# Performance work log

Measured on AMD Instinct MI355X. Metric: run time of the kernel, lower is better.

## Reference

```python
import jax, jax.numpy as jnp
import numpy as np

N, E, IN, H, OUT, K = 50000, 800000, 128, 64, 64, 1024


def setup_inputs() -> dict:
    key = jax.random.key(0)
    ks = jax.random.split(key, 8)
    x = jax.random.normal(ks[0], (N, IN), dtype=jnp.float32)
    edge_index = jax.random.randint(ks[1], (2, E), 0, N, dtype=jnp.int32)
    cluster_id = jax.random.randint(ks[2], (N,), 0, K, dtype=jnp.int32)
    W1 = jax.random.normal(ks[3], (IN, H), dtype=jnp.float32) / np.float32(np.sqrt(IN))
    b1 = jnp.zeros((H,), jnp.float32)
    W2 = jax.random.normal(ks[4], (H, OUT), dtype=jnp.float32) / np.float32(np.sqrt(H))
    b2 = jnp.zeros((OUT,), jnp.float32)
    W_skip = jax.random.normal(ks[5], (H, OUT), dtype=jnp.float32) / np.float32(np.sqrt(H))
    b_skip = jnp.zeros((OUT,), jnp.float32)
    alpha = jnp.full((1,), 1.5, jnp.float32)
    return dict(x=x, edge_index=edge_index, cluster_id=cluster_id, W1=W1, b1=b1,
                W2=W2, b2=b2, W_skip=W_skip, b_skip=b_skip, alpha=alpha)


def gcn_conv_sparse(x, src, dst, n, W, b):
    # PyG GCNConv: transform, then D^{-1/2}(A+I)D^{-1/2} aggregation, then bias.
    h = x @ W  # [n, F_out]
    deg = jax.ops.segment_sum(jnp.ones_like(src, dtype=h.dtype), dst, num_segments=n) + 1.0
    dinv = jax.lax.rsqrt(deg)
    norm = dinv[src] * dinv[dst]  # [E]
    agg = jax.ops.segment_sum(h[src] * norm[:, None], dst, num_segments=n)
    agg = agg + (dinv * dinv)[:, None] * h  # self-loop term
    return agg + b


def reference(x, edge_index, cluster_id, W1, b1, W2, b2, W_skip, b_skip, alpha):
    src, dst = edge_index[0], edge_index[1]
    # conv1 + ReLU (dropout is identity in eval mode)
    x1 = jax.nn.relu(gcn_conv_sparse(x, src, dst, N, W1, b1))  # [N, H]

    # pool_by_partition: scatter-mean node features into K clusters
    sums = jax.ops.segment_sum(x1, cluster_id, num_segments=K)  # [K, H]
    counts = jnp.maximum(jax.ops.segment_sum(jnp.ones((N,), x1.dtype), cluster_id, num_segments=K), 1.0)
    x_p = sums / counts[:, None]

    # deduped pooled edges, self-loops removed == dense 0/1 adjacency with zero diag (K small)
    cu, cv = cluster_id[src], cluster_id[dst]
    A = jnp.zeros((K, K), x1.dtype).at[cu, cv].set(1.0)
    A = A * (1.0 - jnp.eye(K, dtype=x1.dtype))
    A_hat = A + jnp.eye(K, dtype=x1.dtype)
    deg_p = jnp.sum(A_hat, axis=0)  # in-degree at target (PyG computes deg on col)
    dinv_p = jax.lax.rsqrt(deg_p)
    A_norm = dinv_p[:, None] * A_hat * dinv_p[None, :]  # [src, dst]
    h_p = x_p @ W2
    x_p2 = jnp.einsum('st,sf->tf', A_norm, h_p) + b2  # [K, OUT]

    # gather-broadcast + strengthened skip head
    up = x_p2[cluster_id]  # [N, OUT]
    skip = x1 @ W_skip + b_skip
    logits = up + jax.nn.relu(alpha)[0] * skip
    return logits
```

## Files before the change

kernel.cpp:

```cpp
#include <hip/hip_runtime.h>

#define NN 50000
#define NE 800000
#define FIN 128
#define FH 64
#define FOUT 64
#define KC 1024
#define CAP 64

typedef unsigned char  u8;
typedef unsigned short u16;
typedef unsigned int   u32;

__global__ __launch_bounds__(256) void k_edge(const int* __restrict__ src,
                                              const int* __restrict__ dst,
                                              const int* __restrict__ cid,
                                              int* __restrict__ deg,
                                              u16* __restrict__ slots,
                                              u8* __restrict__ AT) {
    int e = blockIdx.x * 256 + threadIdx.x;
    if (e >= NE) return;
    int s = src[e], d = dst[e];
    int pos = atomicAdd(&deg[d], 1);
    if (pos < CAP) slots[(size_t)d * CAP + pos] = (u16)s;
    int cu = cid[s], cv = cid[d];
    if (cu != cv) AT[(size_t)cv * KC + cu] = 1;
}

__global__ __launch_bounds__(256) void k_degp(const u8* __restrict__ AT,
                                              float* __restrict__ dinvp) {
    __shared__ int sm[4];
    int t = blockIdx.x;
    int lane = threadIdx.x & 63, w = threadIdx.x >> 6;
    const u32* row = (const u32*)(AT + (size_t)t * KC);
    int s = __popc(row[threadIdx.x]);
    for (int o = 32; o; o >>= 1) s += __shfl_down(s, o);
    if (lane == 0) sm[w] = s;
    __syncthreads();
    if (threadIdx.x == 0)
        dinvp[t] = rsqrtf(1.0f + (float)(sm[0] + sm[1] + sm[2] + sm[3]));
}

__global__ __launch_bounds__(256) void k_node(const int* __restrict__ deg,
                                              const int* __restrict__ cid,
                                              float* __restrict__ dinv,
                                              int* __restrict__ counts) {
    int i = blockIdx.x * 256 + threadIdx.x;
    if (i >= NN) return;
    dinv[i] = rsqrtf((float)deg[i] + 1.0f);
    atomicAdd(&counts[cid[i]], 1);
}

__global__ __launch_bounds__(256) void k_gemm1(const float* __restrict__ x,
                                               const float* __restrict__ W1,
                                               const float* __restrict__ dinv,
                                               float* __restrict__ h) {
    __shared__ float Ws[FIN * FH];
    __shared__ float Xs[32 * FIN];
    int t = threadIdx.x;
    int row_base = blockIdx.x * 32;
    for (int i = t; i < FIN * FH; i += 256) Ws[i] = W1[i];
    {
        const float4* x4 = (const float4*)x;
        float4* xs4 = (float4*)Xs;
        for (int i = t; i < 32 * 32; i += 256) {
            int r = i >> 5, k4 = i & 31;
            int row = row_base + r;
            float4 v = make_float4(0.f, 0.f, 0.f, 0.f);
            if (row < NN) v = x4[(size_t)row * 32 + k4];
            xs4[i] = v;
        }
    }
    __syncthreads();
    int col = t & 31, grp = t >> 5;
    int r0 = grp * 4;
    const float4* p0 = (const float4*)&Xs[(r0 + 0) * FIN];
    const float4* p1 = (const float4*)&Xs[(r0 + 1) * FIN];
    const float4* p2 = (const float4*)&Xs[(r0 + 2) * FIN];
    const float4* p3 = (const float4*)&Xs[(r0 + 3) * FIN];
    float acc00 = 0.f, acc01 = 0.f, acc10 = 0.f, acc11 = 0.f;
    float acc20 = 0.f, acc21 = 0.f, acc30 = 0.f, acc31 = 0.f;
#pragma unroll 2
    for (int k4 = 0; k4 < FIN / 4; ++k4) {
        float4 a0 = p0[k4], a1 = p1[k4], a2 = p2[k4], a3 = p3[k4];
        const float* wp = &Ws[(k4 * 4) * FH + col];
        float w00 = wp[0],          w01 = wp[32];
        float w10 = wp[FH],         w11 = wp[FH + 32];
        float w20 = wp[2 * FH],     w21 = wp[2 * FH + 32];
        float w30 = wp[3 * FH],     w31 = wp[3 * FH + 32];
        acc00 = fmaf(a0.x, w00, fmaf(a0.y, w10, fmaf(a0.z, w20, fmaf(a0.w, w30, acc00))));
        acc01 = fmaf(a0.x, w01, fmaf(a0.y, w11, fmaf(a0.z, w21, fmaf(a0.w, w31, acc01))));
        acc10 = fmaf(a1.x, w00, fmaf(a1.y, w10, fmaf(a1.z, w20, fmaf(a1.w, w30, acc10))));
        acc11 = fmaf(a1.x, w01, fmaf(a1.y, w11, fmaf(a1.z, w21, fmaf(a1.w, w31, acc11))));
        acc20 = fmaf(a2.x, w00, fmaf(a2.y, w10, fmaf(a2.z, w20, fmaf(a2.w, w30, acc20))));
        acc21 = fmaf(a2.x, w01, fmaf(a2.y, w11, fmaf(a2.z, w21, fmaf(a2.w, w31, acc21))));
        acc30 = fmaf(a3.x, w00, fmaf(a3.y, w10, fmaf(a3.z, w20, fmaf(a3.w, w30, acc30))));
        acc31 = fmaf(a3.x, w01, fmaf(a3.y, w11, fmaf(a3.z, w21, fmaf(a3.w, w31, acc31))));
    }
    int row0 = row_base + r0;
    if (row0 + 0 < NN) { float di = dinv[row0 + 0]; h[(size_t)(row0 + 0) * FH + col] = di * acc00; h[(size_t)(row0 + 0) * FH + col + 32] = di * acc01; }
    if (row0 + 1 < NN) { float di = dinv[row0 + 1]; h[(size_t)(row0 + 1) * FH + col] = di * acc10; h[(size_t)(row0 + 1) * FH + col + 32] = di * acc11; }
    if (row0 + 2 < NN) { float di = dinv[row0 + 2]; h[(size_t)(row0 + 2) * FH + col] = di * acc20; h[(size_t)(row0 + 2) * FH + col + 32] = di * acc21; }
    if (row0 + 3 < NN) { float di = dinv[row0 + 3]; h[(size_t)(row0 + 3) * FH + col] = di * acc30; h[(size_t)(row0 + 3) * FH + col + 32] = di * acc31; }
}

__global__ __launch_bounds__(256) void k_gather(const int* __restrict__ deg,
                                                const u16* __restrict__ slots,
                                                const float* __restrict__ dinv,
                                                const float* __restrict__ h,
                                                const float* __restrict__ b1,
                                                const int* __restrict__ cid,
                                                float* __restrict__ x1,
                                                float* __restrict__ sums) {
    int lane = threadIdx.x & 63;
    int node = blockIdx.x * 4 + (threadIdx.x >> 6);
    if (node >= NN) return;
    int q = lane >> 4, fl = lane & 15;
    const float4* h4 = (const float4*)h;
    int cnt_all = min(deg[node], CAP);
    const u16* cp = slots + (size_t)node * CAP;
    float4 acc = make_float4(0.f, 0.f, 0.f, 0.f);
    {
        int cnt = cnt_all;
        int s = (lane < cnt) ? (int)cp[lane] : 0;
        int nFull = cnt >> 2;
        for (int j = 0; j < nFull; ++j) {
            int ss = __shfl(s, j * 4 + q);
            float4 hv = h4[(size_t)ss * 16 + fl];
            acc.x += hv.x; acc.y += hv.y; acc.z += hv.z; acc.w += hv.w;
        }
        int tail = cnt & 3;
        if (tail) {
            int ss = __shfl(s, nFull * 4 + q);
            float m = (q < tail) ? 1.f : 0.f;
            float4 hv = h4[(size_t)ss * 16 + fl];
            acc.x = fmaf(m, hv.x, acc.x);
            acc.y = fmaf(m, hv.y, acc.y);
            acc.z = fmaf(m, hv.z, acc.z);
            acc.w = fmaf(m, hv.w, acc.w);
        }
    }
    acc.x += __shfl_xor(acc.x, 16); acc.y += __shfl_xor(acc.y, 16);
    acc.z += __shfl_xor(acc.z, 16); acc.w += __shfl_xor(acc.w, 16);
    acc.x += __shfl_xor(acc.x, 32); acc.y += __shfl_xor(acc.y, 32);
    acc.z += __shfl_xor(acc.z, 32); acc.w += __shfl_xor(acc.w, 32);
    float di = dinv[node];
    float4 hs = h4[(size_t)node * 16 + fl];
    const float4* b14 = (const float4*)b1;
    float4 bb = b14[fl];
    float4 v;
    v.x = fmaxf(fmaf(di, acc.x + hs.x, bb.x), 0.f);
    v.y = fmaxf(fmaf(di, acc.y + hs.y, bb.y), 0.f);
    v.z = fmaxf(fmaf(di, acc.z + hs.z, bb.z), 0.f);
    v.w = fmaxf(fmaf(di, acc.w + hs.w, bb.w), 0.f);
    if (q == 0) ((float4*)x1)[(size_t)node * 16 + fl] = v;
    int c = cid[node];
    float comp = (q == 0) ? v.x : (q == 1) ? v.y : (q == 2) ? v.z : v.w;
    unsafeAtomicAdd(&sums[(size_t)c * FH + fl * 4 + q], comp);
}

__global__ __launch_bounds__(64) void k_pool(const float* __restrict__ sums,
                                             const int* __restrict__ counts,
                                             const float* __restrict__ W2,
                                             const float* __restrict__ dinvp,
                                             float* __restrict__ g) {
    __shared__ float xp[FH];
    int s = blockIdx.x, f = threadIdx.x;
    float cnt = fmaxf((float)counts[s], 1.0f);
    xp[f] = sums[(size_t)s * FH + f] / cnt;
    __syncthreads();
    float acc = 0.f;
    for (int j = 0; j < FH; ++j) acc = fmaf(xp[j], W2[j * FH + f], acc);
    g[(size_t)s * FH + f] = dinvp[s] * acc;
}

__global__ __launch_bounds__(256) void k_xp2(const u8* __restrict__ AT,
                                             const float* __restrict__ g,
                                             const float* __restrict__ dinvp,
                                             const float* __restrict__ b2,
                                             float* __restrict__ xp2) {
    __shared__ float4 sm4[4][16];
    int t = blockIdx.x;
    int lane = threadIdx.x & 63, w = threadIdx.x >> 6;
    int q = lane >> 4, fl = lane & 15;
    const u32* roww = (const u32*)(AT + (size_t)t * KC);
    const float4* g4 = (const float4*)g;
    float4 acc = make_float4(0.f, 0.f, 0.f, 0.f);
    int wb = w * 64;
    u32 wv = roww[wb + lane];
    for (int j = 0; j < 16; ++j) {
        u32 word = __shfl((int)wv, j * 4 + q);
        int sidx = (wb + j * 4 + q) * 4;
#pragma unroll
        for (int b = 0; b < 4; ++b) {
            float a = (float)((word >> (8 * b)) & 255u);
            float4 gv = g4[(size_t)(sidx + b) * 16 + fl];
            acc.x = fmaf(a, gv.x, acc.x);
            acc.y = fmaf(a, gv.y, acc.y);
            acc.z = fmaf(a, gv.z, acc.z);
            acc.w = fmaf(a, gv.w, acc.w);
        }
    }
    acc.x += __shfl_xor(acc.x, 16); acc.y += __shfl_xor(acc.y, 16);
    acc.z += __shfl_xor(acc.z, 16); acc.w += __shfl_xor(acc.w, 16);
    acc.x += __shfl_xor(acc.x, 32); acc.y += __shfl_xor(acc.y, 32);
    acc.z += __shfl_xor(acc.z, 32); acc.w += __shfl_xor(acc.w, 32);
    if (q == 0) sm4[w][fl] = acc;
    __syncthreads();
    if (threadIdx.x < 16) {
        int f = threadIdx.x;
        float4 a0 = sm4[0][f], a1 = sm4[1][f], a2 = sm4[2][f], a3 = sm4[3][f];
        float4 gs = g4[(size_t)t * 16 + f];
        float dp = dinvp[t];
        const float4* b24 = (const float4*)b2;
        float4 bb = b24[f];
        float4 o;
        o.x = fmaf(dp, a0.x + a1.x + a2.x + a3.x + gs.x, bb.x);
        o.y = fmaf(dp, a0.y + a1.y + a2.y + a3.y + gs.y, bb.y);
        o.z = fmaf(dp, a0.z + a1.z + a2.z + a3.z + gs.z, bb.z);
        o.w = fmaf(dp, a0.w + a1.w + a2.w + a3.w + gs.w, bb.w);
        ((float4*)xp2)[(size_t)t * 16 + f] = o;
    }
}

__global__ __launch_bounds__(256) void k_final(const float* __restrict__ x1,
                                               const float* __restrict__ Wsk,
                                               const float* __restrict__ bsk,
                                               const float* __restrict__ xp2,
                                               const int* __restrict__ cid,
                                               const float* __restrict__ alpha,
                                               float* __restrict__ out) {
    __shared__ float Ws[FH * FOUT];
    __shared__ float Xs[32 * FH];
    int t = threadIdx.x;
    int row_base = blockIdx.x * 32;
    for (int i = t; i < FH * FOUT; i += 256) Ws[i] = Wsk[i];
    {
        const float4* x4 = (const float4*)x1;
        float4* xs4 = (float4*)Xs;
        for (int i = t; i < 32 * 16; i += 256) {
            int r = i >> 4, k4 = i & 15;
            int row = row_base + r;
            float4 v = make_float4(0.f, 0.f, 0.f, 0.f);
            if (row < NN) v = x4[(size_t)row * 16 + k4];
            xs4[i] = v;
        }
    }
    __syncthreads();
    float al = fmaxf(alpha[0], 0.f);
    int col = t & 31, grp = t >> 5;
    int r0 = grp * 4;
    const float4* p0 = (const float4*)&Xs[(r0 + 0) * FH];
    const float4* p1 = (const float4*)&Xs[(r0 + 1) * FH];
    const float4* p2 = (const float4*)&Xs[(r0 + 2) * FH];
    const float4* p3 = (const float4*)&Xs[(r0 + 3) * FH];
    float acc00 = 0.f, acc01 = 0.f, acc10 = 0.f, acc11 = 0.f;
    float acc20 = 0.f, acc21 = 0.f, acc30 = 0.f, acc31 = 0.f;
#pragma unroll 2
    for (int k4 = 0; k4 < FH / 4; ++k4) {
        float4 a0 = p0[k4], a1 = p1[k4], a2 = p2[k4], a3 = p3[k4];
        const float* wp = &Ws[(k4 * 4) * FOUT + col];
        float w00 = wp[0],           w01 = wp[32];
        float w10 = wp[FOUT],        w11 = wp[FOUT + 32];
        float w20 = wp[2 * FOUT],    w21 = wp[2 * FOUT + 32];
        float w30 = wp[3 * FOUT],    w31 = wp[3 * FOUT + 32];
        acc00 = fmaf(a0.x, w00, fmaf(a0.y, w10, fmaf(a0.z, w20, fmaf(a0.w, w30, acc00))));
        acc01 = fmaf(a0.x, w01, fmaf(a0.y, w11, fmaf(a0.z, w21, fmaf(a0.w, w31, acc01))));
        acc10 = fmaf(a1.x, w00, fmaf(a1.y, w10, fmaf(a1.z, w20, fmaf(a1.w, w30, acc10))));
        acc11 = fmaf(a1.x, w01, fmaf(a1.y, w11, fmaf(a1.z, w21, fmaf(a1.w, w31, acc11))));
        acc20 = fmaf(a2.x, w00, fmaf(a2.y, w10, fmaf(a2.z, w20, fmaf(a2.w, w30, acc20))));
        acc21 = fmaf(a2.x, w01, fmaf(a2.y, w11, fmaf(a2.z, w21, fmaf(a2.w, w31, acc21))));
        acc30 = fmaf(a3.x, w00, fmaf(a3.y, w10, fmaf(a3.z, w20, fmaf(a3.w, w30, acc30))));
        acc31 = fmaf(a3.x, w01, fmaf(a3.y, w11, fmaf(a3.z, w21, fmaf(a3.w, w31, acc31))));
    }
    float bb0 = bsk[col], bb1 = bsk[col + 32];
    int row0 = row_base + r0;
#pragma unroll
    for (int i = 0; i < 4; ++i) {
        float a0 = (i == 0) ? acc00 : (i == 1) ? acc10 : (i == 2) ? acc20 : acc30;
        float a1 = (i == 0) ? acc01 : (i == 1) ? acc11 : (i == 2) ? acc21 : acc31;
        int row = row0 + i;
        if (row < NN) {
            int c = cid[row];
            out[(size_t)row * FOUT + col]      = xp2[(size_t)c * FOUT + col]      + al * (a0 + bb0);
            out[(size_t)row * FOUT + col + 32] = xp2[(size_t)c * FOUT + col + 32] + al * (a1 + bb1);
        }
    }
}

extern "C" void kernel_launch(void* const* d_in, const int* in_sizes, int n_in,
                              void* d_out, int out_size, void* d_ws, size_t ws_size,
                              hipStream_t stream) {
    const float* x    = (const float*)d_in[0];
    const int*   ei   = (const int*)d_in[1];
    const int*   cid  = (const int*)d_in[2];
    const float* W1   = (const float*)d_in[3];
    const float* b1   = (const float*)d_in[4];
    const float* W2   = (const float*)d_in[5];
    const float* b2   = (const float*)d_in[6];
    const float* Wsk  = (const float*)d_in[7];
    const float* bsk  = (const float*)d_in[8];
    const float* alpha= (const float*)d_in[9];
    float* out = (float*)d_out;
    const int* src = ei;
    const int* dst = ei + NE;

    char* ws = (char*)d_ws;
    size_t cur = 0;
    auto alloc = [&](size_t nb) { cur = (cur + 255) & ~(size_t)255; size_t o = cur; cur += nb; return o; };
    size_t o_sums = alloc((size_t)KC * FH * 4);
    size_t o_AT   = alloc((size_t)KC * KC);
    size_t o_deg  = alloc((size_t)NN * 4);
    size_t o_cnt  = alloc((size_t)KC * 4);
    size_t zero_bytes = cur;
    size_t o_slot = alloc((size_t)NN * CAP * 2);
    size_t o_x1   = alloc((size_t)NN * FH * 4);
    size_t o_h    = alloc((size_t)NN * FH * 4);
    size_t o_dinv = alloc((size_t)NN * 4);
    size_t o_g    = alloc((size_t)KC * FH * 4);
    size_t o_xp2  = alloc((size_t)KC * FH * 4);
    size_t o_dinvp= alloc((size_t)KC * 4);
    (void)ws_size; (void)in_sizes; (void)n_in; (void)out_size;

    float* sums = (float*)(ws + o_sums);
    u8*    AT   = (u8*)(ws + o_AT);
    int*   deg  = (int*)(ws + o_deg);
    int*   cnt  = (int*)(ws + o_cnt);
    u16*   slot = (u16*)(ws + o_slot);
    float* x1   = (float*)(ws + o_x1);
    float* h    = (float*)(ws + o_h);
    float* dinv = (float*)(ws + o_dinv);
    float* g    = (float*)(ws + o_g);
    float* xp2  = (float*)(ws + o_xp2);
    float* dinvp= (float*)(ws + o_dinvp);

    hipMemsetAsync(d_ws, 0, zero_bytes, stream);

    const int NRB = (NN + 31) / 32;
    k_edge  <<<(NE + 255) / 256, 256, 0, stream>>>(src, dst, cid, deg, slot, AT);
    k_degp  <<<KC, 256, 0, stream>>>(AT, dinvp);
    k_node  <<<(NN + 255) / 256, 256, 0, stream>>>(deg, cid, dinv, cnt);
    k_gemm1 <<<NRB, 256, 0, stream>>>(x, W1, dinv, h);
    k_gather<<<(NN + 3) / 4, 256, 0, stream>>>(deg, slot, dinv, h, b1, cid, x1, sums);
    k_pool  <<<KC, 64, 0, stream>>>(sums, cnt, W2, dinvp, g);
    k_xp2   <<<KC, 256, 0, stream>>>(AT, g, dinvp, b2, xp2);
    k_final <<<NRB, 256, 0, stream>>>(x1, Wsk, bsk, xp2, cid, alpha, out);
}
```

Before: 232.9 us.

## Build per-node edge slots via two-level bucket partition instead of global atomics

```diff
diff --git a/kernel.cpp b/kernel.cpp
--- a/kernel.cpp
+++ b/kernel.cpp
@@ -7,24 +7,125 @@
 #define FOUT 64
 #define KC 1024
 #define CAP 64
+#define EPB 4096
+#define NCH ((NE + EPB - 1) / EPB)
+#define NBK ((NN + 255) / 256)
 
 typedef unsigned char  u8;
 typedef unsigned short u16;
 typedef unsigned int   u32;
 
-__global__ __launch_bounds__(256) void k_edge(const int* __restrict__ src,
+
+__global__ __launch_bounds__(256) void k_count(const int* __restrict__ dst,
+                                               int* __restrict__ bktcnt) {
+    __shared__ int hist[256];
+    int t = threadIdx.x;
+    hist[t] = 0;
+    __syncthreads();
+    int e0 = blockIdx.x * EPB, e1 = min(NE, e0 + EPB);
+    for (int e = e0 + t; e < e1; e += 256)
+        atomicAdd(&hist[dst[e] >> 8], 1);
+    __syncthreads();
+    if (t < NBK && hist[t]) atomicAdd(&bktcnt[t], hist[t]);
+}
+
+__global__ __launch_bounds__(256) void k_bscan(const int* __restrict__ bktcnt,
+                                               int* __restrict__ bases,
+                                               int* __restrict__ gcur) {
+    __shared__ int sm[256];
+    int t = threadIdx.x;
+    int v = (t < NBK) ? bktcnt[t] : 0;
+    sm[t] = v;
+    __syncthreads();
+    for (int o = 1; o < 256; o <<= 1) {
+        int u = (t >= o) ? sm[t - o] : 0;
+        __syncthreads();
+        sm[t] += u;
+        __syncthreads();
+    }
+    if (t < NBK) { int ex = sm[t] - v; bases[t] = ex; gcur[t] = ex; }
+    if (t == NBK) bases[NBK] = sm[255];
+}
+
+__global__ __launch_bounds__(256) void k_part(const int* __restrict__ src,
                                               const int* __restrict__ dst,
                                               const int* __restrict__ cid,
-                                              int* __restrict__ deg,
-                                              u16* __restrict__ slots,
+                                              int* __restrict__ gcur,
+                                              u32* __restrict__ bin,
                                               u8* __restrict__ AT) {
-    int e = blockIdx.x * 256 + threadIdx.x;
-    if (e >= NE) return;
-    int s = src[e], d = dst[e];
-    int pos = atomicAdd(&deg[d], 1);
-    if (pos < CAP) slots[(size_t)d * CAP + pos] = (u16)s;
-    int cu = cid[s], cv = cid[d];
-    if (cu != cv) AT[(size_t)cv * KC + cu] = 1;
+    __shared__ int hist[256], off[256], cur[256], gbase[256];
+    __shared__ u32 sorted[EPB];
+    int t = threadIdx.x;
+    hist[t] = 0; cur[t] = 0;
+    __syncthreads();
+    int e0 = blockIdx.x * EPB, e1 = min(NE, e0 + EPB);
+    for (int e = e0 + t; e < e1; e += 256)
+        atomicAdd(&hist[dst[e] >> 8], 1);
+    __syncthreads();
+    int v = hist[t];
+    off[t] = v;
+    __syncthreads();
+    for (int o = 1; o < 256; o <<= 1) {
+        int u = (t >= o) ? off[t - o] : 0;
+        __syncthreads();
+        off[t] += u;
+        __syncthreads();
+    }
+    int ex = off[t] - v;
+    __syncthreads();
+    off[t] = ex;
+    __syncthreads();
+    for (int e = e0 + t; e < e1; e += 256) {
+        int d = dst[e], s = src[e];
+        int b = d >> 8, local = d & 255;
+        int cu = cid[s], cv = cid[d];
+        if (cu != cv) AT[(size_t)cv * KC + cu] = 1;
+        int p = off[b] + atomicAdd(&cur[b], 1);
+        sorted[p] = ((u32)b << 24) | ((u32)local << 16) | (u32)s;
+    }
+    __syncthreads();
+    if (t < NBK && hist[t]) gbase[t] = atomicAdd(&gcur[t], hist[t]);
+    __syncthreads();
+    int cnt = e1 - e0;
+    for (int i = t; i < cnt; i += 256) {
+        u32 e = sorted[i];
+        int b = e >> 24;
+        bin[gbase[b] + (i - off[b])] = e;
+    }
+}
+
+__global__ __launch_bounds__(256) void k_slots(const int* __restrict__ bases,
+                                               const u32* __restrict__ bin,
+                                               const int* __restrict__ cid,
+                                               int* __restrict__ deg,
+                                               float* __restrict__ dinv,
+                                               int* __restrict__ counts,
+                                               u16* __restrict__ slots) {
+    __shared__ u16 sbuf[256 * CAP];
+    __shared__ int c_lds[256];
+    int t = threadIdx.x, b = blockIdx.x;
+    c_lds[t] = 0;
+    __syncthreads();
+    int s0 = bases[b], s1 = bases[b + 1];
+    for (int i = s0 + t; i < s1; i += 256) {
+        u32 e = bin[i];
+        int local = (e >> 16) & 255;
+        int pos = atomicAdd(&c_lds[local], 1);
+        if (pos < CAP) sbuf[local * CAP + pos] = (u16)(e & 0xffffu);
+    }
+    __syncthreads();
+    int node = b * 256 + t;
+    if (node < NN) {
+        int d = c_lds[t];
+        deg[node] = d;
+        dinv[node] = rsqrtf((float)d + 1.0f);
+        atomicAdd(&counts[cid[node]], 1);
+    }
+    int rows = min(256, NN - b * 256);
+    int n4 = rows * (CAP * 2 / 16);
+    const uint4* sb4 = (const uint4*)sbuf;
+    uint4* gs4 = (uint4*)(slots + (size_t)b * 256 * CAP);
+    for (int j = t; j < n4; j += 256) gs4[j] = sb4[j];
 }
 
 __global__ __launch_bounds__(256) void k_degp(const u8* __restrict__ AT,
@@ -39,16 +140,6 @@
     __syncthreads();
     if (threadIdx.x == 0)
         dinvp[t] = rsqrtf(1.0f + (float)(sm[0] + sm[1] + sm[2] + sm[3]));
-}
-
-__global__ __launch_bounds__(256) void k_node(const int* __restrict__ deg,
-                                              const int* __restrict__ cid,
-                                              float* __restrict__ dinv,
-                                              int* __restrict__ counts) {
-    int i = blockIdx.x * 256 + threadIdx.x;
-    if (i >= NN) return;
-    dinv[i] = rsqrtf((float)deg[i] + 1.0f);
-    atomicAdd(&counts[cid[i]], 1);
 }
 
 __global__ __launch_bounds__(256) void k_gemm1(const float* __restrict__ x,
@@ -117,11 +208,10 @@
     if (node >= NN) return;
     int q = lane >> 4, fl = lane & 15;
     const float4* h4 = (const float4*)h;
-    int cnt_all = min(deg[node], CAP);
+    int cnt = min(deg[node], CAP);
     const u16* cp = slots + (size_t)node * CAP;
     float4 acc = make_float4(0.f, 0.f, 0.f, 0.f);
     {
-        int cnt = cnt_all;
         int s = (lane < cnt) ? (int)cp[lane] : 0;
         int nFull = cnt >> 2;
         for (int j = 0; j < nFull; ++j) {
@@ -310,10 +400,14 @@
     auto alloc = [&](size_t nb) { cur = (cur + 255) & ~(size_t)255; size_t o = cur; cur += nb; return o; };
     size_t o_sums = alloc((size_t)KC * FH * 4);
     size_t o_AT   = alloc((size_t)KC * KC);
+    size_t o_cnt  = alloc((size_t)KC * 4);
+    size_t o_bkt  = alloc((size_t)NBK * 4);
+    size_t zero_bytes = cur;
+    size_t o_base = alloc((size_t)(NBK + 1) * 4);
+    size_t o_gcur = alloc((size_t)NBK * 4);
+    size_t o_bin  = alloc((size_t)NE * 4);
+    size_t o_slot = alloc((size_t)NN * CAP * 2);
     size_t o_deg  = alloc((size_t)NN * 4);
-    size_t o_cnt  = alloc((size_t)KC * 4);
-    size_t zero_bytes = cur;
-    size_t o_slot = alloc((size_t)NN * CAP * 2);
     size_t o_x1   = alloc((size_t)NN * FH * 4);
     size_t o_h    = alloc((size_t)NN * FH * 4);
     size_t o_dinv = alloc((size_t)NN * 4);
@@ -324,9 +418,13 @@
 
     float* sums = (float*)(ws + o_sums);
     u8*    AT   = (u8*)(ws + o_AT);
+    int*   cnt  = (int*)(ws + o_cnt);
+    int*   bkt  = (int*)(ws + o_bkt);
+    int*   base = (int*)(ws + o_base);
+    int*   gcur = (int*)(ws + o_gcur);
+    u32*   bin  = (u32*)(ws + o_bin);
+    u16*   slot = (u16*)(ws + o_slot);
     int*   deg  = (int*)(ws + o_deg);
-    int*   cnt  = (int*)(ws + o_cnt);
-    u16*   slot = (u16*)(ws + o_slot);
     float* x1   = (float*)(ws + o_x1);
     float* h    = (float*)(ws + o_h);
     float* dinv = (float*)(ws + o_dinv);
@@ -337,9 +435,11 @@
     hipMemsetAsync(d_ws, 0, zero_bytes, stream);
 
     const int NRB = (NN + 31) / 32;
-    k_edge  <<<(NE + 255) / 256, 256, 0, stream>>>(src, dst, cid, deg, slot, AT);
+    k_count <<<NCH, 256, 0, stream>>>(dst, bkt);
+    k_bscan <<<1, 256, 0, stream>>>(bkt, base, gcur);
+    k_part  <<<NCH, 256, 0, stream>>>(src, dst, cid, gcur, bin, AT);
+    k_slots <<<NBK, 256, 0, stream>>>(base, bin, cid, deg, dinv, cnt, slot);
     k_degp  <<<KC, 256, 0, stream>>>(AT, dinvp);
-    k_node  <<<(NN + 255) / 256, 256, 0, stream>>>(deg, cid, dinv, cnt);
     k_gemm1 <<<NRB, 256, 0, stream>>>(x, W1, dinv, h);
     k_gather<<<(NN + 3) / 4, 256, 0, stream>>>(deg, slot, dinv, h, b1, cid, x1, sums);
     k_pool  <<<KC, 64, 0, stream>>>(sums, cnt, W2, dinvp, g);
```

New measurement: 221.2 us. -5.0%, faster.
